# Kernel optimization log

Hardware: AMD Instinct MI355X
Metric: run time of the kernel (lower is better)

## Reference

```python
import jax, jax.numpy as jnp
import numpy as np

B, C_IN, C_OUT, H, W = 128, 128, 128, 40, 40
NUM_EXPERTS, TOP_K, EXPAND = 8, 2, 2
C_HID = C_IN * EXPAND


def setup_inputs() -> dict:
    key = jax.random.key(0)
    ks = jax.random.split(key, 6)
    x = jax.random.normal(ks[0], (B, C_IN, H, W), dtype=jnp.float32)
    weights = jax.random.uniform(ks[1], (B, TOP_K), dtype=jnp.float32)
    indices = jax.random.randint(ks[2], (B, TOP_K), 0, NUM_EXPERTS, dtype=jnp.int64)
    # per-expert 1x1 conv params: expand -> SiLU -> project
    W1 = jax.random.normal(ks[3], (NUM_EXPERTS, C_HID, C_IN), dtype=jnp.float32) * (1.0 / np.sqrt(C_IN))
    b1 = jnp.zeros((NUM_EXPERTS, C_HID), dtype=jnp.float32)
    W2 = jax.random.normal(ks[4], (NUM_EXPERTS, C_OUT, C_HID), dtype=jnp.float32) * (1.0 / np.sqrt(C_HID))
    b2 = jnp.zeros((NUM_EXPERTS, C_OUT), dtype=jnp.float32)
    return {"x": x, "weights": weights, "indices": indices,
            "W1": W1, "b1": b1, "W2": W2, "b2": b2}


def reference(x, weights, indices, W1, b1, W2, b2):
    # Combine top-k gate weights per (batch, expert): duplicate expert picks sum,
    # exactly matching the original's per-expert gather + weighted index_add_.
    Bn = x.shape[0]
    E = W1.shape[0]
    gate = jnp.zeros((Bn, E), dtype=x.dtype).at[jnp.arange(Bn)[:, None], indices].add(weights)  # [B, E]
    out = jnp.zeros((Bn, W2.shape[1]) + x.shape[2:], dtype=x.dtype)
    for e in range(E):  # fixed small expert loop
        h = jax.nn.silu(jnp.einsum('bchw,oc->bohw', x, W1[e]) + b1[e][None, :, None, None])
        y = jnp.einsum('bchw,oc->bohw', h, W2[e]) + b2[e][None, :, None, None]
        out = out + y * gate[:, e][:, None, None, None]
    return out
```

## Files before the change

kernel.cpp:

```cpp
#include <hip/hip_runtime.h>

#define BATCH 128
#define CIN   128
#define CHID  256
#define COUT  128
#define HWPX  1600
#define PXT   64
#define NPXT  25

typedef __attribute__((ext_vector_type(8))) short bf16x8;
typedef __attribute__((ext_vector_type(4))) float f32x4;

__device__ __forceinline__ unsigned short f2bf(float f) {
  unsigned int u = __builtin_bit_cast(unsigned int, f);
  u += 0x7FFFu + ((u >> 16) & 1u);
  return (unsigned short)(u >> 16);
}

__device__ __forceinline__ float silu_f(float v) {
  return v / (1.0f + __expf(-v));
}

__global__ __launch_bounds__(256) void convert_w_kernel(
    const float* __restrict__ W1, const float* __restrict__ W2,
    unsigned short* __restrict__ W1b, unsigned short* __restrict__ W2b) {
  int i = blockIdx.x * 256 + threadIdx.x;
  W1b[i] = f2bf(W1[i]);
  W2b[i] = f2bf(W2[i]);
}

__global__ __launch_bounds__(256) void moe_kernel(
    const float* __restrict__ x, const float* __restrict__ wts,
    const int* __restrict__ idx, const unsigned short* __restrict__ W1,
    const float* __restrict__ b1, const unsigned short* __restrict__ W2,
    const float* __restrict__ b2, float* __restrict__ out) {
  __shared__ unsigned short xs[PXT][CIN + 8];
  __shared__ unsigned short hs[PXT][128 + 8];

  const int tid  = threadIdx.x;
  const int wave = tid >> 6;
  const int lane = tid & 63;
  const int q    = lane >> 4;
  const int r16  = lane & 15;

  const int blk = blockIdx.x;
  const int b   = blk / NPXT;
  const int pt  = blk - b * NPXT;
  const int px0 = pt * PXT;

  {
    const float* xb = x + (long)b * CIN * HWPX + px0;
    const int prow = tid >> 4;
    const int ppx  = (tid & 15) * 4;
#pragma unroll
    for (int it = 0; it < 8; ++it) {
      const int cin = it * 16 + prow;
      const float4 v = *reinterpret_cast<const float4*>(xb + (long)cin * HWPX + ppx);
      xs[ppx + 0][cin] = f2bf(v.x);
      xs[ppx + 1][cin] = f2bf(v.y);
      xs[ppx + 2][cin] = f2bf(v.z);
      xs[ppx + 3][cin] = f2bf(v.w);
    }
  }
  __syncthreads();

  f32x4 accO[2][4];
#pragma unroll
  for (int mt = 0; mt < 2; ++mt)
#pragma unroll
    for (int nt = 0; nt < 4; ++nt) accO[mt][nt] = (f32x4){0.f, 0.f, 0.f, 0.f};

  for (int slot = 0; slot < 2; ++slot) {
    const int   e = idx[b * 2 + slot];
    const float g = wts[b * 2 + slot];
    const unsigned short* W1e = W1 + (long)e * CHID * CIN;
    const unsigned short* W2e = W2 + (long)e * COUT * CHID;
    const float* b1e = b1 + e * CHID;

    f32x4 acc2[2][4];
#pragma unroll
    for (int mt = 0; mt < 2; ++mt)
#pragma unroll
      for (int nt = 0; nt < 4; ++nt) acc2[mt][nt] = (f32x4){0.f, 0.f, 0.f, 0.f};

#pragma unroll
    for (int half = 0; half < 2; ++half) {
      f32x4 acc1[2][4];
#pragma unroll
      for (int mt = 0; mt < 2; ++mt)
#pragma unroll
        for (int nt = 0; nt < 4; ++nt) acc1[mt][nt] = (f32x4){0.f, 0.f, 0.f, 0.f};

#pragma unroll
      for (int ks = 0; ks < 4; ++ks) {
        const int kofs = ks * 32 + q * 8;
        const int row0 = half * 128 + wave * 32 + r16;
        const bf16x8 a0 = *reinterpret_cast<const bf16x8*>(W1e + (row0) * CIN + kofs);
        const bf16x8 a1 = *reinterpret_cast<const bf16x8*>(W1e + (row0 + 16) * CIN + kofs);
        bf16x8 bb[4];
#pragma unroll
        for (int nt = 0; nt < 4; ++nt)
          bb[nt] = *reinterpret_cast<const bf16x8*>(&xs[nt * 16 + r16][kofs]);
#pragma unroll
        for (int nt = 0; nt < 4; ++nt) {
          acc1[0][nt] = __builtin_amdgcn_mfma_f32_16x16x32_bf16(a0, bb[nt], acc1[0][nt], 0, 0, 0);
          acc1[1][nt] = __builtin_amdgcn_mfma_f32_16x16x32_bf16(a1, bb[nt], acc1[1][nt], 0, 0, 0);
        }
      }

#pragma unroll
      for (int mt = 0; mt < 2; ++mt) {
        const int chh = wave * 32 + mt * 16 + q * 4;
        const f32x4 bias = *reinterpret_cast<const f32x4*>(b1e + half * 128 + chh);
#pragma unroll
        for (int nt = 0; nt < 4; ++nt) {
          const f32x4 v = acc1[mt][nt] + bias;
          const unsigned int lo = (unsigned int)f2bf(silu_f(v[0])) |
                                  ((unsigned int)f2bf(silu_f(v[1])) << 16);
          const unsigned int hi = (unsigned int)f2bf(silu_f(v[2])) |
                                  ((unsigned int)f2bf(silu_f(v[3])) << 16);
          *reinterpret_cast<uint2*>(&hs[nt * 16 + r16][chh]) = make_uint2(lo, hi);
        }
      }
      __syncthreads();

#pragma unroll
      for (int ks = 0; ks < 4; ++ks) {
        const int kofs = ks * 32 + q * 8;
        const int row0 = wave * 32 + r16;
        const bf16x8 a0 = *reinterpret_cast<const bf16x8*>(W2e + (row0) * CHID + half * 128 + kofs);
        const bf16x8 a1 = *reinterpret_cast<const bf16x8*>(W2e + (row0 + 16) * CHID + half * 128 + kofs);
        bf16x8 bb[4];
#pragma unroll
        for (int nt = 0; nt < 4; ++nt)
          bb[nt] = *reinterpret_cast<const bf16x8*>(&hs[nt * 16 + r16][kofs]);
#pragma unroll
        for (int nt = 0; nt < 4; ++nt) {
          acc2[0][nt] = __builtin_amdgcn_mfma_f32_16x16x32_bf16(a0, bb[nt], acc2[0][nt], 0, 0, 0);
          acc2[1][nt] = __builtin_amdgcn_mfma_f32_16x16x32_bf16(a1, bb[nt], acc2[1][nt], 0, 0, 0);
        }
      }
      __syncthreads();
    }

    const float* b2e = b2 + e * COUT;
#pragma unroll
    for (int mt = 0; mt < 2; ++mt) {
      const f32x4 bias2 = *reinterpret_cast<const f32x4*>(b2e + wave * 32 + mt * 16 + q * 4);
#pragma unroll
      for (int nt = 0; nt < 4; ++nt) accO[mt][nt] += g * (acc2[mt][nt] + bias2);
    }
  }

  const long ob = (long)b * COUT * HWPX + px0;
#pragma unroll
  for (int mt = 0; mt < 2; ++mt) {
    const int co = wave * 32 + mt * 16 + q * 4;
#pragma unroll
    for (int nt = 0; nt < 4; ++nt) {
      const int px = nt * 16 + r16;
#pragma unroll
      for (int r = 0; r < 4; ++r)
        out[ob + (long)(co + r) * HWPX + px] = accO[mt][nt][r];
    }
  }
}

extern "C" void kernel_launch(void* const* d_in, const int* in_sizes, int n_in,
                              void* d_out, int out_size, void* d_ws, size_t ws_size,
                              hipStream_t stream) {
  const float* x   = (const float*)d_in[0];
  const float* wts = (const float*)d_in[1];
  const int*   idx = (const int*)d_in[2];
  const float* W1  = (const float*)d_in[3];
  const float* b1  = (const float*)d_in[4];
  const float* W2  = (const float*)d_in[5];
  const float* b2  = (const float*)d_in[6];
  float* out = (float*)d_out;

  unsigned short* W1b = (unsigned short*)d_ws;
  unsigned short* W2b = (unsigned short*)d_ws + (8 * CHID * CIN);

  convert_w_kernel<<<262144 / 256, 256, 0, stream>>>(W1, W2, W1b, W2b);

  moe_kernel<<<BATCH * NPXT, 256, 0, stream>>>(x, wts, idx, W1b, b1, W2b, b2, out);
}
```

Before: 307.8 us.

## Keep hidden activations in registers by permuting W1 rows to match MFMA layout

W1 rows are permuted during weight conversion so the first GEMM's accumulator layout lines up with the B-operand fragment of the second GEMM. Each wave now owns 16 pixels and streams all 256 hidden channels in groups of 32, feeding SiLU output straight into the W2 MFMA without going through shared memory. This drops the hs buffer and the per-half __syncthreads, and the gate weight is folded into h before the second GEMM. In exchange each wave now reads every W1/W2 fragment from global/L2 for only 16 pixels, so weight reuse per load drops, and the bias b1 read layout depends on the permutation being correct.

```diff
diff --git a/kernel.cpp b/kernel.cpp
--- a/kernel.cpp
+++ b/kernel.cpp
@@ -1,6 +1,5 @@
 #include <hip/hip_runtime.h>
 
-#define BATCH 128
 #define CIN   128
 #define CHID  256
 #define COUT  128
@@ -25,8 +24,16 @@
     const float* __restrict__ W1, const float* __restrict__ W2,
     unsigned short* __restrict__ W1b, unsigned short* __restrict__ W2b) {
   int i = blockIdx.x * 256 + threadIdx.x;
-  W1b[i] = f2bf(W1[i]);
   W2b[i] = f2bf(W2[i]);
+  int c = i % CIN;
+  int p = (i / CIN) % CHID;
+  int e = i / (CIN * CHID);
+  int g  = p >> 5;
+  int pp = p & 31;
+  int mt = pp >> 4;
+  int row = pp & 15;
+  int ch = (g << 5) + ((row >> 2) << 3) + (row & 3) + (mt << 2);
+  W1b[i] = f2bf(W1[(e * CHID + ch) * CIN + c]);
 }
 
 __global__ __launch_bounds__(256) void moe_kernel(
@@ -35,7 +42,6 @@
     const float* __restrict__ b1, const unsigned short* __restrict__ W2,
     const float* __restrict__ b2, float* __restrict__ out) {
   __shared__ unsigned short xs[PXT][CIN + 8];
-  __shared__ unsigned short hs[PXT][128 + 8];
 
   const int tid  = threadIdx.x;
   const int wave = tid >> 6;
@@ -50,119 +56,84 @@
 
   {
     const float* xb = x + (long)b * CIN * HWPX + px0;
-    const int prow = tid >> 4;
-    const int ppx  = (tid & 15) * 4;
+    const int pxl = tid & 63;
+    const int cb  = tid >> 6;
 #pragma unroll
-    for (int it = 0; it < 8; ++it) {
-      const int cin = it * 16 + prow;
-      const float4 v = *reinterpret_cast<const float4*>(xb + (long)cin * HWPX + ppx);
-      xs[ppx + 0][cin] = f2bf(v.x);
-      xs[ppx + 1][cin] = f2bf(v.y);
-      xs[ppx + 2][cin] = f2bf(v.z);
-      xs[ppx + 3][cin] = f2bf(v.w);
+    for (int i = 0; i < 4; ++i) {
+      const int cin0 = cb * 32 + i * 8;
+      bf16x8 v;
+#pragma unroll
+      for (int j = 0; j < 8; ++j)
+        v[j] = (short)f2bf(xb[(cin0 + j) * HWPX + pxl]);
+      *reinterpret_cast<bf16x8*>(&xs[pxl][cin0]) = v;
     }
   }
   __syncthreads();
 
-  f32x4 accO[2][4];
+  bf16x8 xfrag[4];
 #pragma unroll
-  for (int mt = 0; mt < 2; ++mt)
+  for (int ks = 0; ks < 4; ++ks)
+    xfrag[ks] = *reinterpret_cast<const bf16x8*>(&xs[wave * 16 + r16][ks * 32 + q * 8]);
+
+  f32x4 accO[8];
 #pragma unroll
-    for (int nt = 0; nt < 4; ++nt) accO[mt][nt] = (f32x4){0.f, 0.f, 0.f, 0.f};
+  for (int mt = 0; mt < 8; ++mt) accO[mt] = (f32x4){0.f, 0.f, 0.f, 0.f};
+
+  const int   e0 = idx[b * 2 + 0], e1 = idx[b * 2 + 1];
+  const float g0 = wts[b * 2 + 0], g1 = wts[b * 2 + 1];
 
   for (int slot = 0; slot < 2; ++slot) {
-    const int   e = idx[b * 2 + slot];
-    const float g = wts[b * 2 + slot];
+    const int   e = slot ? e1 : e0;
+    const float g = slot ? g1 : g0;
     const unsigned short* W1e = W1 + (long)e * CHID * CIN;
     const unsigned short* W2e = W2 + (long)e * COUT * CHID;
     const float* b1e = b1 + e * CHID;
 
-    f32x4 acc2[2][4];
-#pragma unroll
-    for (int mt = 0; mt < 2; ++mt)
-#pragma unroll
-      for (int nt = 0; nt < 4; ++nt) acc2[mt][nt] = (f32x4){0.f, 0.f, 0.f, 0.f};
+    for (int grp = 0; grp < 8; ++grp) {
+      const int base = grp * 32;
 
-#pragma unroll
-    for (int half = 0; half < 2; ++half) {
-      f32x4 acc1[2][4];
-#pragma unroll
-      for (int mt = 0; mt < 2; ++mt)
-#pragma unroll
-        for (int nt = 0; nt < 4; ++nt) acc1[mt][nt] = (f32x4){0.f, 0.f, 0.f, 0.f};
-
+      f32x4 aA = (f32x4){0.f, 0.f, 0.f, 0.f};
+      f32x4 aB = (f32x4){0.f, 0.f, 0.f, 0.f};
 #pragma unroll
       for (int ks = 0; ks < 4; ++ks) {
-        const int kofs = ks * 32 + q * 8;
-        const int row0 = half * 128 + wave * 32 + r16;
-        const bf16x8 a0 = *reinterpret_cast<const bf16x8*>(W1e + (row0) * CIN + kofs);
-        const bf16x8 a1 = *reinterpret_cast<const bf16x8*>(W1e + (row0 + 16) * CIN + kofs);
-        bf16x8 bb[4];
+        const bf16x8 w0 = *reinterpret_cast<const bf16x8*>(
+            W1e + (base + r16) * CIN + ks * 32 + q * 8);
+        const bf16x8 w1 = *reinterpret_cast<const bf16x8*>(
+            W1e + (base + 16 + r16) * CIN + ks * 32 + q * 8);
+        aA = __builtin_amdgcn_mfma_f32_16x16x32_bf16(w0, xfrag[ks], aA, 0, 0, 0);
+        aB = __builtin_amdgcn_mfma_f32_16x16x32_bf16(w1, xfrag[ks], aB, 0, 0, 0);
+      }
+
+      const f32x4 bA = *reinterpret_cast<const f32x4*>(&b1e[base + q * 8]);
+      const f32x4 bB = *reinterpret_cast<const f32x4*>(&b1e[base + q * 8 + 4]);
+      bf16x8 h;
 #pragma unroll
-        for (int nt = 0; nt < 4; ++nt)
-          bb[nt] = *reinterpret_cast<const bf16x8*>(&xs[nt * 16 + r16][kofs]);
-#pragma unroll
-        for (int nt = 0; nt < 4; ++nt) {
-          acc1[0][nt] = __builtin_amdgcn_mfma_f32_16x16x32_bf16(a0, bb[nt], acc1[0][nt], 0, 0, 0);
-          acc1[1][nt] = __builtin_amdgcn_mfma_f32_16x16x32_bf16(a1, bb[nt], acc1[1][nt], 0, 0, 0);
-        }
+      for (int j = 0; j < 4; ++j) {
+        h[j]     = (short)f2bf(g * silu_f(aA[j] + bA[j]));
+        h[4 + j] = (short)f2bf(g * silu_f(aB[j] + bB[j]));
       }
 
 #pragma unroll
-      for (int mt = 0; mt < 2; ++mt) {
-        const int chh = wave * 32 + mt * 16 + q * 4;
-        const f32x4 bias = *reinterpret_cast<const f32x4*>(b1e + half * 128 + chh);
-#pragma unroll
-        for (int nt = 0; nt < 4; ++nt) {
-          const f32x4 v = acc1[mt][nt] + bias;
-          const unsigned int lo = (unsigned int)f2bf(silu_f(v[0])) |
-                                  ((unsigned int)f2bf(silu_f(v[1])) << 16);
-          const unsigned int hi = (unsigned int)f2bf(silu_f(v[2])) |
-                                  ((unsigned int)f2bf(silu_f(v[3])) << 16);
-          *reinterpret_cast<uint2*>(&hs[nt * 16 + r16][chh]) = make_uint2(lo, hi);
-        }
+      for (int mt = 0; mt < 8; ++mt) {
+        const bf16x8 w2 = *reinterpret_cast<const bf16x8*>(
+            W2e + (mt * 16 + r16) * CHID + base + q * 8);
+        accO[mt] = __builtin_amdgcn_mfma_f32_16x16x32_bf16(w2, h, accO[mt], 0, 0, 0);
       }
-      __syncthreads();
-
-#pragma unroll
-      for (int ks = 0; ks < 4; ++ks) {
-        const int kofs = ks * 32 + q * 8;
-        const int row0 = wave * 32 + r16;
-        const bf16x8 a0 = *reinterpret_cast<const bf16x8*>(W2e + (row0) * CHID + half * 128 + kofs);
-        const bf16x8 a1 = *reinterpret_cast<const bf16x8*>(W2e + (row0 + 16) * CHID + half * 128 + kofs);
-        bf16x8 bb[4];
-#pragma unroll
-        for (int nt = 0; nt < 4; ++nt)
-          bb[nt] = *reinterpret_cast<const bf16x8*>(&hs[nt * 16 + r16][kofs]);
-#pragma unroll
-        for (int nt = 0; nt < 4; ++nt) {
-          acc2[0][nt] = __builtin_amdgcn_mfma_f32_16x16x32_bf16(a0, bb[nt], acc2[0][nt], 0, 0, 0);
-          acc2[1][nt] = __builtin_amdgcn_mfma_f32_16x16x32_bf16(a1, bb[nt], acc2[1][nt], 0, 0, 0);
-        }
-      }
-      __syncthreads();
-    }
-
-    const float* b2e = b2 + e * COUT;
-#pragma unroll
-    for (int mt = 0; mt < 2; ++mt) {
-      const f32x4 bias2 = *reinterpret_cast<const f32x4*>(b2e + wave * 32 + mt * 16 + q * 4);
-#pragma unroll
-      for (int nt = 0; nt < 4; ++nt) accO[mt][nt] += g * (acc2[mt][nt] + bias2);
     }
   }
 
-  const long ob = (long)b * COUT * HWPX + px0;
+  const float* b2e0 = b2 + e0 * COUT;
+  const float* b2e1 = b2 + e1 * COUT;
+  const long ob = (long)b * COUT * HWPX + px0 + wave * 16 + r16;
 #pragma unroll
-  for (int mt = 0; mt < 2; ++mt) {
-    const int co = wave * 32 + mt * 16 + q * 4;
+  for (int mt = 0; mt < 8; ++mt) {
+    const int co = mt * 16 + q * 4;
+    const f32x4 v = accO[mt] +
+                    g0 * (*reinterpret_cast<const f32x4*>(&b2e0[co])) +
+                    g1 * (*reinterpret_cast<const f32x4*>(&b2e1[co]));
 #pragma unroll
-    for (int nt = 0; nt < 4; ++nt) {
-      const int px = nt * 16 + r16;
-#pragma unroll
-      for (int r = 0; r < 4; ++r)
-        out[ob + (long)(co + r) * HWPX + px] = accO[mt][nt][r];
-    }
+    for (int r = 0; r < 4; ++r)
+      out[ob + (long)(co + r) * HWPX] = v[r];
   }
 }
 
@@ -182,6 +153,5 @@
   unsigned short* W2b = (unsigned short*)d_ws + (8 * CHID * CIN);
 
   convert_w_kernel<<<262144 / 256, 256, 0, stream>>>(W1, W2, W1b, W2b);
-
-  moe_kernel<<<BATCH * NPXT, 256, 0, stream>>>(x, wts, idx, W1b, b1, W2b, b2, out);
+  moe_kernel<<<128 * NPXT, 256, 0, stream>>>(x, wts, idx, W1b, b1, W2b, b2, out);
 }
```

Result: slower. 587.6 us (+90.9%).
